# Kernel tuning notes

Measured on AMD Instinct MI355X. Metric: run time of the kernel, lower is better.

The kernel has to match this reference:

```python
import jax, jax.numpy as jnp
import numpy as np
import math

B, S, D = 4, 2048, 1024
H, HD = 16, 64
RANK = 16
SCALING = 32.0 / RANK  # alpha / rank = 2.0


def setup_inputs() -> dict:
    key = jax.random.key(0)
    ks = jax.random.split(key, 12)
    s = 1.0 / math.sqrt(D)
    inp = {
        "hidden_states": jax.random.normal(ks[0], (B, S, D), dtype=jnp.float32),
        "attention_mask": jnp.zeros((B, 1, 1, S), dtype=jnp.float32),
        "Wq": jax.random.normal(ks[1], (D, D), dtype=jnp.float32) * s,
        "bq": jnp.zeros((D,), dtype=jnp.float32),
        "Aq": jax.random.normal(ks[2], (RANK, D), dtype=jnp.float32) * s,
        "Bq": jax.random.normal(ks[3], (D, RANK), dtype=jnp.float32) * 0.02,
        "Wk": jax.random.normal(ks[4], (D, D), dtype=jnp.float32) * s,
        "bk": jnp.zeros((D,), dtype=jnp.float32),
        "Wv": jax.random.normal(ks[5], (D, D), dtype=jnp.float32) * s,
        "bv": jnp.zeros((D,), dtype=jnp.float32),
        "Av": jax.random.normal(ks[6], (RANK, D), dtype=jnp.float32) * s,
        "Bv": jax.random.normal(ks[7], (D, RANK), dtype=jnp.float32) * 0.02,
        "Wo": jax.random.normal(ks[8], (D, D), dtype=jnp.float32) * s,
        "bo": jnp.zeros((D,), dtype=jnp.float32),
    }
    return inp


def _lora_linear(x, W, b, A, Bm):
    # F.linear(x, W, b) + (x @ A.T @ B.T) * scaling
    return x @ W.T + b + ((x @ A.T) @ Bm.T) * SCALING


def reference(hidden_states, attention_mask, Wq, bq, Aq, Bq, Wk, bk, Wv, bv, Av, Bv, Wo, bo):
    x = hidden_states
    q = _lora_linear(x, Wq, bq, Aq, Bq)          # [B,S,D]
    k = x @ Wk.T + bk                             # [B,S,D]
    v = _lora_linear(x, Wv, bv, Av, Bv)           # [B,S,D]

    def split_heads(t):
        return t.reshape(B, S, H, HD).transpose(0, 2, 1, 3)  # [B,H,S,HD]

    q, k, v = split_heads(q), split_heads(k), split_heads(v)
    scores = jnp.einsum("bhqd,bhkd->bhqk", q, k) / math.sqrt(HD)  # [B,H,S,S]
    scores = scores + attention_mask
    attn = jax.nn.softmax(scores, axis=-1)
    ctx = jnp.einsum("bhqk,bhkd->bhqd", attn, v)  # [B,H,S,HD]
    ctx = ctx.transpose(0, 2, 1, 3).reshape(B, S, D)
    return ctx @ Wo.T + bo
```

## Files before the change

### kernel.cpp

```cpp
#include <hip/hip_runtime.h>
#include <cstdint>


#define D_DIM 1024
#define S_DIM 2048
#define B_DIM 4
#define H_DIM 16
#define HD_DIM 64
#define M_DIM 8192
#define LOG2E 1.44269504f

typedef __bf16 bf16;
typedef __bf16 bf16x4v __attribute__((ext_vector_type(4)));
typedef __bf16 bf16x8 __attribute__((ext_vector_type(8)));
typedef float f32x4 __attribute__((ext_vector_type(4)));

typedef __attribute__((address_space(1))) void* as1p;
typedef __attribute__((address_space(3))) void* as3p;

__device__ __forceinline__ void gll16(const void* g, void* l) {
  __builtin_amdgcn_global_load_lds((as1p)(g), (as3p)(l), 16, 0, 0);
}

__global__ void convert_x_kernel(const float* __restrict__ x, bf16* __restrict__ xb) {
  const int i = (blockIdx.x * 256 + threadIdx.x) * 8;
  const float4 a = *(const float4*)(x + i);
  const float4 b = *(const float4*)(x + i + 4);
  bf16x8 o;
  o[0] = (bf16)a.x; o[1] = (bf16)a.y; o[2] = (bf16)a.z; o[3] = (bf16)a.w;
  o[4] = (bf16)b.x; o[5] = (bf16)b.y; o[6] = (bf16)b.z; o[7] = (bf16)b.w;
  *(bf16x8*)(xb + i) = o;
}

__global__ void prep_w_kernel(const float* __restrict__ W, const float* __restrict__ A,
                              const float* __restrict__ Bm, bf16* __restrict__ out,
                              int use_lora) {
  const int i = blockIdx.x * 256 + threadIdx.x;
  const int n = i >> 10, k = i & (D_DIM - 1);
  float w = W[i];
  if (use_lora) {
    float acc = 0.f;
#pragma unroll
    for (int r = 0; r < 16; ++r) acc = fmaf(Bm[n * 16 + r], A[r * D_DIM + k], acc);
    w += 2.0f * acc;
  }
  out[i] = (bf16)w;
}

__global__ __launch_bounds__(256) void gemm_qkv_kernel(
    const bf16* __restrict__ X, const bf16* __restrict__ Wqkv,
    const float* __restrict__ bq, const float* __restrict__ bk,
    const float* __restrict__ bv, bf16* __restrict__ Qo, bf16* __restrict__ Ko,
    bf16* __restrict__ Vo) {
  __shared__ __attribute__((aligned(16))) bf16 As[2][128 * 64];
  __shared__ __attribute__((aligned(16))) bf16 Bs[2][128 * 64];
  const int tid = threadIdx.x;
  const int wave = tid >> 6, lane = tid & 63;
  const int quad = lane >> 4, l16 = lane & 15;
  const int m0 = blockIdx.x * 128, n0 = blockIdx.y * 128;
  const int wm = (wave >> 1) * 64, wn = (wave & 1) * 64;
  const int srow = lane >> 3, sblk = lane & 7;

  const f32x4 zero = {0.f, 0.f, 0.f, 0.f};
  f32x4 acc[4][4];
#pragma unroll
  for (int mi = 0; mi < 4; ++mi)
#pragma unroll
    for (int ni = 0; ni < 4; ++ni) acc[mi][ni] = zero;

  auto stage = [&](int kt) {
    const int buf = kt & 1, kb = kt * 64;
#pragma unroll
    for (int it = 0; it < 4; ++it) {
      const int c = it * 4 + wave;
      const int row = c * 8 + srow;
      const int b = sblk ^ (row & 7);
      gll16(X + (size_t)(m0 + row) * D_DIM + kb + b * 8, &As[buf][c * 512 + lane * 8]);
      gll16(Wqkv + (size_t)(n0 + row) * D_DIM + kb + b * 8, &Bs[buf][c * 512 + lane * 8]);
    }
  };
  stage(0);

  for (int kt = 0; kt < D_DIM / 64; ++kt) {
    __syncthreads();
    if (kt + 1 < D_DIM / 64) stage(kt + 1);
    const bf16* as_ = &As[kt & 1][0];
    const bf16* bs_ = &Bs[kt & 1][0];
#pragma unroll
    for (int ks = 0; ks < 2; ++ks) {
      bf16x8 af[4], bfr[4];
#pragma unroll
      for (int mi = 0; mi < 4; ++mi) {
        const int row = wm + mi * 16 + l16;
        af[mi] = *(const bf16x8*)(as_ + row * 64 + (((ks * 4 + quad) ^ (row & 7)) * 8));
      }
#pragma unroll
      for (int ni = 0; ni < 4; ++ni) {
        const int row = wn + ni * 16 + l16;
        bfr[ni] = *(const bf16x8*)(bs_ + row * 64 + (((ks * 4 + quad) ^ (row & 7)) * 8));
      }
#pragma unroll
      for (int mi = 0; mi < 4; ++mi)
#pragma unroll
        for (int ni = 0; ni < 4; ++ni)
          acc[mi][ni] =
              __builtin_amdgcn_mfma_f32_16x16x32_bf16(af[mi], bfr[ni], acc[mi][ni], 0, 0, 0);
    }
  }

  const int sel = n0 >> 10;
  const float* bp = (sel == 0) ? bq : (sel == 1) ? bk : bv;
  const float qs = 0.125f * LOG2E;

  if (sel == 2) {
#pragma unroll
    for (int ni = 0; ni < 4; ++ni) {
      const int c = (n0 + wn + ni * 16 + l16) & 1023;
      const int h = c >> 6, hd = c & 63;
      const float bvv = bp[c];
#pragma unroll
      for (int mi = 0; mi < 4; ++mi) {
        const int row0 = m0 + wm + mi * 16 + quad * 4;
        const int b = row0 >> 11, s0 = row0 & (S_DIM - 1);
        bf16x4v pk;
#pragma unroll
        for (int r = 0; r < 4; ++r) pk[r] = (bf16)(acc[mi][ni][r] + bvv);
        *(bf16x4v*)(Vo + ((size_t)(b * H_DIM + h) * HD_DIM + hd) * S_DIM + s0) = pk;
      }
    }
  } else {
    bf16* O = (sel == 0) ? Qo : Ko;
#pragma unroll
    for (int ni = 0; ni < 4; ++ni) {
      const int c = (n0 + wn + ni * 16 + l16) & 1023;
      const int h = c >> 6, hd = c & 63;
      const float bvv = bp[c];
#pragma unroll
      for (int mi = 0; mi < 4; ++mi) {
#pragma unroll
        for (int r = 0; r < 4; ++r) {
          const int row = m0 + wm + mi * 16 + quad * 4 + r;
          const int b = row >> 11, s = row & (S_DIM - 1);
          float v = acc[mi][ni][r] + bvv;
          if (sel == 0) v *= qs;
          O[((size_t)(b * H_DIM + h) * S_DIM + s) * HD_DIM + hd] = (bf16)v;
        }
      }
    }
  }
}

__global__ __launch_bounds__(256) void gemm_o_kernel(const bf16* __restrict__ X,
                                                     const bf16* __restrict__ W,
                                                     const float* __restrict__ bias,
                                                     float* __restrict__ out) {
  __shared__ __attribute__((aligned(16))) bf16 As[2][128 * 64];
  __shared__ __attribute__((aligned(16))) bf16 Bs[2][128 * 64];
  const int tid = threadIdx.x;
  const int wave = tid >> 6, lane = tid & 63;
  const int quad = lane >> 4, l16 = lane & 15;
  const int m0 = blockIdx.x * 128, n0 = blockIdx.y * 128;
  const int wm = (wave >> 1) * 64, wn = (wave & 1) * 64;
  const int srow = lane >> 3, sblk = lane & 7;

  const f32x4 zero = {0.f, 0.f, 0.f, 0.f};
  f32x4 acc[4][4];
#pragma unroll
  for (int mi = 0; mi < 4; ++mi)
#pragma unroll
    for (int ni = 0; ni < 4; ++ni) acc[mi][ni] = zero;

  auto stage = [&](int kt) {
    const int buf = kt & 1, kb = kt * 64;
#pragma unroll
    for (int it = 0; it < 4; ++it) {
      const int c = it * 4 + wave;
      const int row = c * 8 + srow;
      const int b = sblk ^ (row & 7);
      gll16(X + (size_t)(m0 + row) * D_DIM + kb + b * 8, &As[buf][c * 512 + lane * 8]);
      gll16(W + (size_t)(n0 + row) * D_DIM + kb + b * 8, &Bs[buf][c * 512 + lane * 8]);
    }
  };
  stage(0);

  for (int kt = 0; kt < D_DIM / 64; ++kt) {
    __syncthreads();
    if (kt + 1 < D_DIM / 64) stage(kt + 1);
    const bf16* as_ = &As[kt & 1][0];
    const bf16* bs_ = &Bs[kt & 1][0];
#pragma unroll
    for (int ks = 0; ks < 2; ++ks) {
      bf16x8 af[4], bfr[4];
#pragma unroll
      for (int mi = 0; mi < 4; ++mi) {
        const int row = wm + mi * 16 + l16;
        af[mi] = *(const bf16x8*)(as_ + row * 64 + (((ks * 4 + quad) ^ (row & 7)) * 8));
      }
#pragma unroll
      for (int ni = 0; ni < 4; ++ni) {
        const int row = wn + ni * 16 + l16;
        bfr[ni] = *(const bf16x8*)(bs_ + row * 64 + (((ks * 4 + quad) ^ (row & 7)) * 8));
      }
#pragma unroll
      for (int mi = 0; mi < 4; ++mi)
#pragma unroll
        for (int ni = 0; ni < 4; ++ni)
          acc[mi][ni] =
              __builtin_amdgcn_mfma_f32_16x16x32_bf16(af[mi], bfr[ni], acc[mi][ni], 0, 0, 0);
    }
  }
#pragma unroll
  for (int ni = 0; ni < 4; ++ni) {
    const int col = n0 + wn + ni * 16 + l16;
    const float bv = bias[col];
#pragma unroll
    for (int mi = 0; mi < 4; ++mi)
#pragma unroll
      for (int r = 0; r < 4; ++r) {
        const int row = m0 + wm + mi * 16 + quad * 4 + r;
        out[(size_t)row * D_DIM + col] = acc[mi][ni][r] + bv;
      }
  }
}

__global__ __launch_bounds__(256, 2) void attn_kernel(const bf16* __restrict__ Q,
                                                      const bf16* __restrict__ K,
                                                      const bf16* __restrict__ Vt,
                                                      const float* __restrict__ mask,
                                                      bf16* __restrict__ ctx) {
  __shared__ __attribute__((aligned(16))) bf16 Ks[2][64 * 64];
  __shared__ __attribute__((aligned(16))) bf16 Vs[2][64 * 64];
  __shared__ __attribute__((aligned(16))) bf16 Ps[4][64 * 64];
  __shared__ __attribute__((aligned(16))) float cms[S_DIM];

  const int tid = threadIdx.x;
  const int wave = tid >> 6, lane = tid & 63;
  const int quad = lane >> 4, l16 = lane & 15;
  const int bh = blockIdx.y, b = bh >> 4, h = bh & 15;
  const int qt = blockIdx.x;

  const bf16* Qg = Q + ((size_t)bh * S_DIM + qt * 256 + wave * 64) * HD_DIM;
  bf16x8 qf[4][2];
#pragma unroll
  for (int nq = 0; nq < 4; ++nq)
#pragma unroll
    for (int ks = 0; ks < 2; ++ks)
      qf[nq][ks] = *(const bf16x8*)(Qg + (nq * 16 + l16) * HD_DIM + ks * 32 + quad * 8);

  {
    const float* mp = mask + b * S_DIM + tid * 8;
    const float4 a = *(const float4*)(mp);
    const float4 c = *(const float4*)(mp + 4);
    f32x4 r0 = {fmaf(a.x, LOG2E, -16.f), fmaf(a.y, LOG2E, -16.f),
                fmaf(a.z, LOG2E, -16.f), fmaf(a.w, LOG2E, -16.f)};
    f32x4 r1 = {fmaf(c.x, LOG2E, -16.f), fmaf(c.y, LOG2E, -16.f),
                fmaf(c.z, LOG2E, -16.f), fmaf(c.w, LOG2E, -16.f)};
    *(f32x4*)(cms + tid * 8) = r0;
    *(f32x4*)(cms + tid * 8 + 4) = r1;
  }

  bf16x8 onef;
#pragma unroll
  for (int j = 0; j < 8; ++j) onef[j] = (bf16)1.0f;

  const f32x4 zero = {0.f, 0.f, 0.f, 0.f};
  f32x4 o[4][4], osum[4];
#pragma unroll
  for (int nq = 0; nq < 4; ++nq) {
    osum[nq] = zero;
#pragma unroll
    for (int nh = 0; nh < 4; ++nh) o[nq][nh] = zero;
  }

  const bf16* Kg0 = K + (size_t)bh * S_DIM * HD_DIM;
  const bf16* Vg0 = Vt + (size_t)bh * HD_DIM * S_DIM;

  auto stage = [&](int t) {
    const int buf = t & 1;
    const bf16* Kg = Kg0 + (size_t)t * 64 * HD_DIM;
    const bf16* Vg = Vg0 + t * 64;
#pragma unroll
    for (int it = 0; it < 2; ++it) {
      const int c = it * 4 + wave;
      const int row = c * 8 + (lane >> 3);
      const int blk = (lane & 7) ^ (row & 7);
      gll16(Kg + (size_t)row * HD_DIM + blk * 8, &Ks[buf][c * 512 + lane * 8]);
      gll16(Vg + (size_t)row * S_DIM + blk * 8, &Vs[buf][c * 512 + lane * 8]);
    }
  };
  stage(0);

  bf16* pw = &Ps[wave][0];
  for (int t = 0; t < S_DIM / 64; ++t) {
    __syncthreads();
    if (t + 1 < S_DIM / 64) stage(t + 1);
    const bf16* ks_ = &Ks[t & 1][0];
    const bf16* vs_ = &Vs[t & 1][0];

#pragma unroll
    for (int mt = 0; mt < 4; ++mt) {
      f32x4 sc[4];
#pragma unroll
      for (int nq = 0; nq < 4; ++nq) sc[nq] = zero;
#pragma unroll
      for (int ks = 0; ks < 2; ++ks) {
        const int row = mt * 16 + l16;
        const bf16x8 kf =
            *(const bf16x8*)(ks_ + row * 64 + (((ks * 4 + quad) ^ (row & 7)) * 8));
#pragma unroll
        for (int nq = 0; nq < 4; ++nq)
          sc[nq] = __builtin_amdgcn_mfma_f32_16x16x32_bf16(kf, qf[nq][ks], sc[nq], 0, 0, 0);
      }
      const f32x4 cm = *(const f32x4*)(cms + t * 64 + mt * 16 + quad * 4);
      const int kvblk = mt * 2 + (quad >> 1);
#pragma unroll
      for (int nq = 0; nq < 4; ++nq) {
        bf16x4v pk;
#pragma unroll
        for (int r = 0; r < 4; ++r) pk[r] = (bf16)exp2f(sc[nq][r] + cm[r]);
        const int q = nq * 16 + l16;
        *(bf16x4v*)(pw + q * 64 + ((kvblk ^ (q & 7)) * 8) + (quad & 1) * 4) = pk;
      }
    }

#pragma unroll
    for (int ks = 0; ks < 2; ++ks) {
      bf16x8 pf[4];
#pragma unroll
      for (int nq = 0; nq < 4; ++nq) {
        const int q = nq * 16 + l16;
        pf[nq] = *(const bf16x8*)(pw + q * 64 + (((ks * 4 + quad) ^ (q & 7)) * 8));
      }
#pragma unroll
      for (int nh = 0; nh < 4; ++nh) {
        const int vrow = nh * 16 + l16;
        const bf16x8 vf =
            *(const bf16x8*)(vs_ + vrow * 64 + (((ks * 4 + quad) ^ (vrow & 7)) * 8));
#pragma unroll
        for (int nq = 0; nq < 4; ++nq)
          o[nq][nh] = __builtin_amdgcn_mfma_f32_16x16x32_bf16(pf[nq], vf, o[nq][nh], 0, 0, 0);
      }
#pragma unroll
      for (int nq = 0; nq < 4; ++nq)
        osum[nq] = __builtin_amdgcn_mfma_f32_16x16x32_bf16(pf[nq], onef, osum[nq], 0, 0, 0);
    }
  }

#pragma unroll
  for (int nq = 0; nq < 4; ++nq)
#pragma unroll
    for (int r = 0; r < 4; ++r) {
      const float inv = 1.0f / osum[nq][r];
      const int s = qt * 256 + wave * 64 + nq * 16 + quad * 4 + r;
#pragma unroll
      for (int nh = 0; nh < 4; ++nh)
        ctx[((size_t)b * S_DIM + s) * D_DIM + h * 64 + nh * 16 + l16] =
            (bf16)(o[nq][nh][r] * inv);
    }
}

extern "C" void kernel_launch(void* const* d_in, const int* in_sizes, int n_in,
                              void* d_out, int out_size, void* d_ws, size_t ws_size,
                              hipStream_t stream) {
  const float* x    = (const float*)d_in[0];
  const float* mask = (const float*)d_in[1];
  const float* Wq   = (const float*)d_in[2];
  const float* bq   = (const float*)d_in[3];
  const float* Aq   = (const float*)d_in[4];
  const float* Bq   = (const float*)d_in[5];
  const float* Wk   = (const float*)d_in[6];
  const float* bk   = (const float*)d_in[7];
  const float* Wv   = (const float*)d_in[8];
  const float* bv   = (const float*)d_in[9];
  const float* Av   = (const float*)d_in[10];
  const float* Bv   = (const float*)d_in[11];
  const float* Wo   = (const float*)d_in[12];
  const float* bo   = (const float*)d_in[13];
  float* out = (float*)d_out;

  bf16* xb   = (bf16*)d_ws;
  bf16* wqkv = xb + (size_t)M_DIM * D_DIM;
  bf16* wo   = wqkv + (size_t)3 * D_DIM * D_DIM;
  bf16* Qw   = wo + (size_t)D_DIM * D_DIM;
  bf16* Kw   = Qw + (size_t)M_DIM * D_DIM;
  bf16* Vw   = Kw + (size_t)M_DIM * D_DIM;
  bf16* Cw   = xb;

  convert_x_kernel<<<M_DIM * D_DIM / (256 * 8), 256, 0, stream>>>(x, xb);
  prep_w_kernel<<<D_DIM * D_DIM / 256, 256, 0, stream>>>(Wq, Aq, Bq, wqkv, 1);
  prep_w_kernel<<<D_DIM * D_DIM / 256, 256, 0, stream>>>(Wk, nullptr, nullptr,
                                                         wqkv + (size_t)D_DIM * D_DIM, 0);
  prep_w_kernel<<<D_DIM * D_DIM / 256, 256, 0, stream>>>(Wv, Av, Bv,
                                                         wqkv + (size_t)2 * D_DIM * D_DIM, 1);
  prep_w_kernel<<<D_DIM * D_DIM / 256, 256, 0, stream>>>(Wo, nullptr, nullptr, wo, 0);

  gemm_qkv_kernel<<<dim3(M_DIM / 128, 3 * D_DIM / 128), 256, 0, stream>>>(
      xb, wqkv, bq, bk, bv, Qw, Kw, Vw);

  attn_kernel<<<dim3(S_DIM / 256, B_DIM * H_DIM), 256, 0, stream>>>(Qw, Kw, Vw, mask, Cw);

  gemm_o_kernel<<<dim3(M_DIM / 128, D_DIM / 128), 256, 0, stream>>>(Cw, wo, bo, out);
}
```

Baseline: 332.0 us.

## Keep attention probabilities in registers via permlane swaps instead of LDS

The attention kernel no longer writes the exponentiated score tile P to per-wave shared memory and reads it back. It packs the bf16 probabilities in registers and rearranges them into the MFMA A-operand layout with permlane32/permlane16 swaps, processing the key tile in two halves. It also switches to the raw hardware exp2 intrinsic. This removes LDS traffic and 32KB of shared memory per block, which may allow higher occupancy, at the cost of extra cross-lane ops and register pressure.

```diff
diff --git a/kernel.cpp b/kernel.cpp
--- a/kernel.cpp
+++ b/kernel.cpp
@@ -11,6 +11,8 @@
 #define LOG2E 1.44269504f
 
 typedef __bf16 bf16;
+typedef unsigned int u32;
+typedef __bf16 bf16x2v __attribute__((ext_vector_type(2)));
 typedef __bf16 bf16x4v __attribute__((ext_vector_type(4)));
 typedef __bf16 bf16x8 __attribute__((ext_vector_type(8)));
 typedef float f32x4 __attribute__((ext_vector_type(4)));
@@ -20,6 +22,13 @@
 
 __device__ __forceinline__ void gll16(const void* g, void* l) {
   __builtin_amdgcn_global_load_lds((as1p)(g), (as3p)(l), 16, 0, 0);
+}
+
+__device__ __forceinline__ u32 pack_bf16(float lo, float hi) {
+  bf16x2v t;
+  t[0] = (bf16)lo;
+  t[1] = (bf16)hi;
+  return __builtin_bit_cast(u32, t);
 }
 
 __global__ void convert_x_kernel(const float* __restrict__ x, bf16* __restrict__ xb) {
@@ -230,7 +239,6 @@
                                                       bf16* __restrict__ ctx) {
   __shared__ __attribute__((aligned(16))) bf16 Ks[2][64 * 64];
   __shared__ __attribute__((aligned(16))) bf16 Vs[2][64 * 64];
-  __shared__ __attribute__((aligned(16))) bf16 Ps[4][64 * 64];
   __shared__ __attribute__((aligned(16))) float cms[S_DIM];
 
   const int tid = threadIdx.x;
@@ -290,7 +298,6 @@
   };
   stage(0);
 
-  bf16* pw = &Ps[wave][0];
   for (int t = 0; t < S_DIM / 64; ++t) {
     __syncthreads();
     if (t + 1 < S_DIM / 64) stage(t + 1);
@@ -298,51 +305,62 @@
     const bf16* vs_ = &Vs[t & 1][0];
 
 #pragma unroll
-    for (int mt = 0; mt < 4; ++mt) {
-      f32x4 sc[4];
-#pragma unroll
-      for (int nq = 0; nq < 4; ++nq) sc[nq] = zero;
-#pragma unroll
-      for (int ks = 0; ks < 2; ++ks) {
-        const int row = mt * 16 + l16;
-        const bf16x8 kf =
-            *(const bf16x8*)(ks_ + row * 64 + (((ks * 4 + quad) ^ (row & 7)) * 8));
-#pragma unroll
-        for (int nq = 0; nq < 4; ++nq)
-          sc[nq] = __builtin_amdgcn_mfma_f32_16x16x32_bf16(kf, qf[nq][ks], sc[nq], 0, 0, 0);
-      }
-      const f32x4 cm = *(const f32x4*)(cms + t * 64 + mt * 16 + quad * 4);
-      const int kvblk = mt * 2 + (quad >> 1);
-#pragma unroll
-      for (int nq = 0; nq < 4; ++nq) {
-        bf16x4v pk;
-#pragma unroll
-        for (int r = 0; r < 4; ++r) pk[r] = (bf16)exp2f(sc[nq][r] + cm[r]);
-        const int q = nq * 16 + l16;
-        *(bf16x4v*)(pw + q * 64 + ((kvblk ^ (q & 7)) * 8) + (quad & 1) * 4) = pk;
-      }
-    }
-
-#pragma unroll
-    for (int ks = 0; ks < 2; ++ks) {
-      bf16x8 pf[4];
-#pragma unroll
-      for (int nq = 0; nq < 4; ++nq) {
-        const int q = nq * 16 + l16;
-        pf[nq] = *(const bf16x8*)(pw + q * 64 + (((ks * 4 + quad) ^ (q & 7)) * 8));
-      }
+    for (int half = 0; half < 2; ++half) {
+      u32 pk[4][2][2];
+#pragma unroll
+      for (int mtl = 0; mtl < 2; ++mtl) {
+        const int mt = half * 2 + mtl;
+        f32x4 sc[4];
+#pragma unroll
+        for (int nq = 0; nq < 4; ++nq) sc[nq] = zero;
+#pragma unroll
+        for (int ks = 0; ks < 2; ++ks) {
+          const int row = mt * 16 + l16;
+          const bf16x8 kf =
+              *(const bf16x8*)(ks_ + row * 64 + (((ks * 4 + quad) ^ (row & 7)) * 8));
+#pragma unroll
+          for (int nq = 0; nq < 4; ++nq)
+            sc[nq] = __builtin_amdgcn_mfma_f32_16x16x32_bf16(kf, qf[nq][ks], sc[nq], 0, 0, 0);
+        }
+        const f32x4 cm = *(const f32x4*)(cms + t * 64 + mt * 16 + quad * 4);
+#pragma unroll
+        for (int nq = 0; nq < 4; ++nq) {
+          const float e0 = __builtin_amdgcn_exp2f(sc[nq][0] + cm[0]);
+          const float e1 = __builtin_amdgcn_exp2f(sc[nq][1] + cm[1]);
+          const float e2 = __builtin_amdgcn_exp2f(sc[nq][2] + cm[2]);
+          const float e3 = __builtin_amdgcn_exp2f(sc[nq][3] + cm[3]);
+          pk[nq][mtl][0] = pack_bf16(e0, e1);
+          pk[nq][mtl][1] = pack_bf16(e2, e3);
+        }
+      }
+
+      bf16x8 vf[4];
 #pragma unroll
       for (int nh = 0; nh < 4; ++nh) {
         const int vrow = nh * 16 + l16;
-        const bf16x8 vf =
-            *(const bf16x8*)(vs_ + vrow * 64 + (((ks * 4 + quad) ^ (vrow & 7)) * 8));
-#pragma unroll
-        for (int nq = 0; nq < 4; ++nq)
-          o[nq][nh] = __builtin_amdgcn_mfma_f32_16x16x32_bf16(pf[nq], vf, o[nq][nh], 0, 0, 0);
-      }
-#pragma unroll
-      for (int nq = 0; nq < 4; ++nq)
-        osum[nq] = __builtin_amdgcn_mfma_f32_16x16x32_bf16(pf[nq], onef, osum[nq], 0, 0, 0);
+        vf[nh] = *(const bf16x8*)(vs_ + vrow * 64 + (((half * 4 + quad) ^ (vrow & 7)) * 8));
+      }
+
+#pragma unroll
+      for (int nq = 0; nq < 4; ++nq) {
+        auto a0 = __builtin_amdgcn_permlane32_swap(pk[nq][0][0], pk[nq][1][0], false, false);
+        auto a1 = __builtin_amdgcn_permlane32_swap(pk[nq][0][1], pk[nq][1][1], false, false);
+        auto b0 = __builtin_amdgcn_permlane16_swap(a0[0], a0[1], false, false);
+        auto b1 = __builtin_amdgcn_permlane16_swap(a1[0], a1[1], false, false);
+        union {
+          u32 w[4];
+          bf16x8 v;
+        } pu;
+        pu.w[0] = b0[0];
+        pu.w[1] = b1[0];
+        pu.w[2] = b0[1];
+        pu.w[3] = b1[1];
+        const bf16x8 pf = pu.v;
+#pragma unroll
+        for (int nh = 0; nh < 4; ++nh)
+          o[nq][nh] = __builtin_amdgcn_mfma_f32_16x16x32_bf16(pf, vf[nh], o[nq][nh], 0, 0, 0);
+        osum[nq] = __builtin_amdgcn_mfma_f32_16x16x32_bf16(pf, onef, osum[nq], 0, 0, 0);
+      }
     }
   }
 
```

Measured after the change: 303.6 us. 1.09x faster.
